# Kernel tuning notes

Measured on AMD Instinct MI355X. Metric: run time of the kernel, lower is better.

The kernel has to match this reference:

```python
import jax, jax.numpy as jnp
import numpy as np

NMS_THR = 0.7
TOPK = 128      # fixed post-NMS rois per level (static padding for jit)
OUT = 14        # RoIAlign output size
SAMPLES = 2     # samples per bin per dim (fixed approximation of sampling_ratio=-1)
STRIDES = (32.0, 16.0, 8.0)


def get_channel(a):
    # a: [..., 4] boxes as (cx, cy, w, h); FPN level assignment, clamped to [1, 4]
    s = jnp.sqrt(a[..., 2] * a[..., 3])
    return jnp.clip(jnp.floor(3.0 + jnp.log2(s / 224.0)), 1.0, 4.0)


def cxcywh_to_xyxy(b):
    cx, cy, w, h = b[..., 0], b[..., 1], b[..., 2], b[..., 3]
    return jnp.stack([cx - w / 2, cy - h / 2, cx + w / 2, cy + h / 2], axis=-1)


def pairwise_iou(b):
    x1, y1, x2, y2 = b[:, 0], b[:, 1], b[:, 2], b[:, 3]
    area = jnp.maximum(x2 - x1, 0.0) * jnp.maximum(y2 - y1, 0.0)
    ix1 = jnp.maximum(x1[:, None], x1[None, :])
    iy1 = jnp.maximum(y1[:, None], y1[None, :])
    ix2 = jnp.minimum(x2[:, None], x2[None, :])
    iy2 = jnp.minimum(y2[:, None], y2[None, :])
    inter = jnp.maximum(ix2 - ix1, 0.0) * jnp.maximum(iy2 - iy1, 0.0)
    union = area[:, None] + area[None, :] - inter
    return inter / jnp.maximum(union, 1e-9)


def nms_keep(boxes_xyxy, scores, thr):
    # Greedy NMS over masked scores (-inf entries sort last and are excluded later).
    n = scores.shape[0]
    order = jnp.argsort(-scores)
    iou = pairwise_iou(boxes_xyxy[order])  # [N, N]
    idx = jnp.arange(n)

    def body(sup, i):
        keep_i = ~sup[i]
        sup = sup | (keep_i & (iou[i] > thr) & (idx > i))
        return sup, keep_i

    _, keeps_sorted = jax.lax.scan(body, jnp.zeros(n, dtype=bool), idx)
    return jnp.zeros(n, dtype=bool).at[order].set(keeps_sorted)


def roi_align(feat, boxes):
    # feat: [C, H, W]; boxes: [K, 4]. NOTE: the original prepare_boxes feeds
    # (cx, cy, w, h) straight into RoIAlign, which interprets them as
    # (x1, y1, x2, y2) -- replicated faithfully here. spatial_scale = 1.
    C, H, W = feat.shape
    K = boxes.shape[0]
    x1, y1, x2, y2 = boxes[:, 0], boxes[:, 1], boxes[:, 2], boxes[:, 3]
    rw = jnp.maximum(x2 - x1, 1.0)
    rh = jnp.maximum(y2 - y1, 1.0)
    bw = rw / OUT
    bh = rh / OUT
    # fractional bin offsets, [OUT*SAMPLES]
    f = (jnp.arange(OUT, dtype=feat.dtype)[:, None]
         + (jnp.arange(SAMPLES, dtype=feat.dtype)[None, :] + 0.5) / SAMPLES).reshape(-1)
    ys = y1[:, None] + bh[:, None] * f[None, :]  # [K, S]
    xs = x1[:, None] + bw[:, None] * f[None, :]
    Y = ys[:, :, None]  # [K, S, 1]
    X = xs[:, None, :]  # [K, 1, S]
    valid = (Y > -1.0) & (Y < H) & (X > -1.0) & (X < W)  # [K, S, S]
    Yc = jnp.clip(Y, 0.0, H - 1.0)
    Xc = jnp.clip(X, 0.0, W - 1.0)
    y0 = jnp.floor(Yc)
    x0 = jnp.floor(Xc)
    y0i = y0.astype(jnp.int32)
    x0i = x0.astype(jnp.int32)
    y1i = jnp.minimum(y0i + 1, H - 1)
    x1i = jnp.minimum(x0i + 1, W - 1)
    ly = Yc - y0
    lx = Xc - x0
    hy = 1.0 - ly
    hx = 1.0 - lx
    g = lambda yi, xi: feat[:, yi, xi]  # -> [C, K, S, S]
    val = (g(y0i, x0i) * (hy * hx) + g(y0i, x1i) * (hy * lx)
           + g(y1i, x0i) * (ly * hx) + g(y1i, x1i) * (ly * lx))
    val = val * valid.astype(val.dtype)
    val = val.reshape(C, K, OUT, SAMPLES, OUT, SAMPLES).mean(axis=(3, 5))
    return jnp.transpose(val, (1, 0, 2, 3))  # [K, C, OUT, OUT]


def level_extract(feat, boxes, scores, levs, nl):
    # one image, one target FPN level: mask, NMS, fixed top-K select, RoIAlign
    mask = levs == nl
    msc = jnp.where(mask, scores, -jnp.inf)
    xyxy = cxcywh_to_xyxy(boxes)
    keep = nms_keep(jax.lax.stop_gradient(xyxy), jax.lax.stop_gradient(msc), NMS_THR)
    eff = jnp.where(keep & mask, msc, -jnp.inf)
    vals, sel = jax.lax.top_k(jax.lax.stop_gradient(eff), TOPK)
    valid = jnp.isfinite(vals)
    rois = boxes[sel] * valid[:, None].astype(boxes.dtype)
    out = roi_align(feat, rois)
    return out * valid[:, None, None, None].astype(out.dtype)


def _forward(p32, p16, p8, p4, a32, a16, a8, s32, s16, s8):
    anchors = (a32, a16, a8)  # p4 proposals are computed then discarded in the
    # original (grouping loop only runs l in range(3)); p4 features are never
    # RoIAligned either (nl loops 1..3), so p4 only appears as an unused input.
    levs = jnp.concatenate([get_channel(a) for a in anchors], axis=1)      # [B, N]
    boxes = jnp.concatenate([a * s for a, s in zip(anchors, STRIDES)], axis=1)
    scores = jnp.concatenate([s32, s16, s8], axis=1)
    outs = []
    for nl, feat in zip((1.0, 2.0, 3.0), (p32, p16, p8)):
        fn = jax.vmap(lambda f, b, s, l, nl=nl: level_extract(f, b, s, l, nl))
        outs.append(fn(feat, boxes, scores, levs))  # [B, TOPK, C, 14, 14]
    return jnp.concatenate(outs, axis=1)  # [B, 3*TOPK, C, 14, 14]


def setup_inputs():
    key = jax.random.key(0)
    ks = jax.random.split(key, 10)
    B, C = 2, 256
    p32 = jax.random.normal(ks[0], (B, C, 32, 32), jnp.float32)
    p16 = jax.random.normal(ks[1], (B, C, 64, 64), jnp.float32)
    p8 = jax.random.normal(ks[2], (B, C, 128, 128), jnp.float32)
    p4 = jax.random.normal(ks[3], (B, C, 256, 256), jnp.float32)

    def mk_anchors(k, n, hf):
        k1, k2 = jax.random.split(k)
        cxy = jax.random.uniform(k1, (B, n, 2), jnp.float32) * hf
        wh = 16.0 + jax.random.uniform(k2, (B, n, 2), jnp.float32) * 434.0
        return jnp.concatenate([cxy, wh], axis=-1)

    anchors_32 = mk_anchors(ks[4], 512, 32.0)
    anchors_16 = mk_anchors(ks[5], 1024, 64.0)
    anchors_8 = mk_anchors(ks[6], 2048, 128.0)
    scores_32 = jax.random.normal(ks[7], (B, 512), jnp.float32)
    scores_16 = jax.random.normal(ks[8], (B, 1024), jnp.float32)
    scores_8 = jax.random.normal(ks[9], (B, 2048), jnp.float32)
    return dict(p32=p32, p16=p16, p8=p8, p4=p4,
                anchors_32=anchors_32, anchors_16=anchors_16, anchors_8=anchors_8,
                scores_32=scores_32, scores_16=scores_16, scores_8=scores_8)


def reference(p32, p16, p8, p4, anchors_32, anchors_16, anchors_8,
              scores_32, scores_16, scores_8):
    return _forward(p32, p16, p8, p4, anchors_32, anchors_16, anchors_8,
                    scores_32, scores_16, scores_8)
```

## Files before the change

### kernel.cpp

```cpp
#include <hip/hip_runtime.h>
#include <stdint.h>

#define NMS_THR 0.7f
#define TOPK 128
#define NTOT 3584
#define CAP 2048
#define OUTSZ 14
#define NSAMP 28

typedef unsigned long long u64;
typedef float vf4 __attribute__((ext_vector_type(4)));
typedef float float2u __attribute__((ext_vector_type(2), aligned(4)));

__device__ __forceinline__ void fetch_anchor(
    const float* __restrict__ a32, const float* __restrict__ a16,
    const float* __restrict__ a8,
    const float* __restrict__ s32, const float* __restrict__ s16,
    const float* __restrict__ s8,
    int b, int i, float* A, float* st, float* sc)
{
    const float* P;
    if (i < 512) {
        P = a32 + (b * 512 + i) * 4;  *st = 32.0f; *sc = s32[b * 512 + i];
    } else if (i < 1536) {
        int j = i - 512;
        P = a16 + (b * 1024 + j) * 4; *st = 16.0f; *sc = s16[b * 1024 + j];
    } else {
        int j = i - 1536;
        P = a8 + (b * 2048 + j) * 4;  *st = 8.0f;  *sc = s8[b * 2048 + j];
    }
    float4 v = *(const float4*)P;
    A[0] = v.x; A[1] = v.y; A[2] = v.z; A[3] = v.w;
}

__global__ __launch_bounds__(1024) void select_kernel(
    const float* __restrict__ a32, const float* __restrict__ a16,
    const float* __restrict__ a8,
    const float* __restrict__ s32, const float* __restrict__ s16,
    const float* __restrict__ s8,
    float* __restrict__ rois,
    int* __restrict__ validOut)
{
    __shared__ u64 key[CAP];
    __shared__ float cbox[CAP * 5];
    __shared__ float kbox[TOPK * 5];
    __shared__ u64 supmat[64];
    __shared__ unsigned extf[64];
    __shared__ int selList[TOPK];
    __shared__ int mCount, keptSh;

    int prob = blockIdx.x;
    int b = prob / 3;
    int nl = prob % 3 + 1;
    int tid = threadIdx.x;

    if (tid == 0) { mCount = 0; keptSh = 0; }
    __syncthreads();

    for (int i = tid; i < NTOT; i += 1024) {
        float A[4], st, sc;
        fetch_anchor(a32, a16, a8, s32, s16, s8, b, i, A, &st, &sc);
        float s = sqrtf(__fmul_rn(A[2], A[3]));
        float lv = floorf(__fadd_rn(3.0f, log2f(__fdiv_rn(s, 224.0f))));
        lv = fminf(fmaxf(lv, 1.0f), 4.0f);
        if ((int)lv == nl) {
            unsigned u = __float_as_uint(sc);
            u = (u & 0x80000000u) ? ~u : (u | 0x80000000u);
            unsigned d = ~u;
            int pos = atomicAdd(&mCount, 1);
            if (pos < CAP) key[pos] = ((u64)d << 32) | (unsigned)i;
        }
    }
    __syncthreads();
    int m = mCount;
    if (m > CAP) m = CAP;
    int P2 = 64;
    while (P2 < m) P2 <<= 1;
    for (int i = m + tid; i < P2; i += 1024) key[i] = ~0ull;
    __syncthreads();

    for (int k = 2; k <= P2; k <<= 1) {
        for (int j = k >> 1; j > 0; j >>= 1) {
            for (int t = tid; t < P2; t += 1024) {
                int ixj = t ^ j;
                if (ixj > t) {
                    u64 a = key[t], bb = key[ixj];
                    bool up = ((t & k) == 0);
                    if ((a > bb) == up) { key[t] = bb; key[ixj] = a; }
                }
            }
            __syncthreads();
        }
    }

    for (int r = tid; r < m; r += 1024) {
        int orig = (int)(key[r] & 0xffffffffu);
        float A[4], st, sc;
        fetch_anchor(a32, a16, a8, s32, s16, s8, b, orig, A, &st, &sc);
        float cx = A[0] * st, cy = A[1] * st, w = A[2] * st, h = A[3] * st;
        float x1 = __fsub_rn(cx, 0.5f * w);
        float y1 = __fsub_rn(cy, 0.5f * h);
        float x2 = __fadd_rn(cx, 0.5f * w);
        float y2 = __fadd_rn(cy, 0.5f * h);
        cbox[r * 5 + 0] = x1; cbox[r * 5 + 1] = y1;
        cbox[r * 5 + 2] = x2; cbox[r * 5 + 3] = y2;
        cbox[r * 5 + 4] = __fmul_rn(fmaxf(__fsub_rn(x2, x1), 0.0f),
                                    fmaxf(__fsub_rn(y2, y1), 0.0f));
    }
    __syncthreads();

    int lane = tid & 63;
    int wv = tid >> 6;
    int kept = 0;

    for (int base = 0; base < m && kept < TOPK; base += 64) {
        int n = m - base; if (n > 64) n = 64;
        if (tid < 64) extf[tid] = 0;
        __syncthreads();

        bool cvalid = lane < n;
        int cidx = (base + (cvalid ? lane : 0)) * 5;
        float cx1 = cbox[cidx], cy1 = cbox[cidx + 1];
        float cx2 = cbox[cidx + 2], cy2 = cbox[cidx + 3], car = cbox[cidx + 4];

        for (int k = wv; k < kept; k += 16) {
            float kx1 = kbox[k * 5], ky1 = kbox[k * 5 + 1];
            float kx2 = kbox[k * 5 + 2], ky2 = kbox[k * 5 + 3], kar = kbox[k * 5 + 4];
            float i1 = fmaxf(kx1, cx1), i2 = fmaxf(ky1, cy1);
            float i3 = fminf(kx2, cx2), i4 = fminf(ky2, cy2);
            float inr = __fmul_rn(fmaxf(__fsub_rn(i3, i1), 0.0f),
                                  fmaxf(__fsub_rn(i4, i2), 0.0f));
            float unr = __fsub_rn(__fadd_rn(kar, car), inr);
            if (cvalid && __fdiv_rn(inr, fmaxf(unr, 1e-9f)) > NMS_THR)
                atomicOr(&extf[lane], 1u);
        }

        for (int r = 0; r < 4; r++) {
            int i = wv * 4 + r;
            u64 bal = 0;
            if (i < n) {
                int iidx = (base + i) * 5;
                float ix1 = cbox[iidx], iy1 = cbox[iidx + 1];
                float ix2 = cbox[iidx + 2], iy2 = cbox[iidx + 3], iar = cbox[iidx + 4];
                float i1 = fmaxf(ix1, cx1), i2 = fmaxf(iy1, cy1);
                float i3 = fminf(ix2, cx2), i4 = fminf(iy2, cy2);
                float inr = __fmul_rn(fmaxf(__fsub_rn(i3, i1), 0.0f),
                                      fmaxf(__fsub_rn(i4, i2), 0.0f));
                float unr = __fsub_rn(__fadd_rn(iar, car), inr);
                bool bit = cvalid && (lane > i) &&
                           (__fdiv_rn(inr, fmaxf(unr, 1e-9f)) > NMS_THR);
                bal = __ballot(bit);
            }
            if (lane == 0) supmat[i] = bal;
        }
        __syncthreads();

        if (wv == 0) {
            u64 row = supmat[lane];
            bool alive = (lane < n) && (extf[lane] == 0);
            int nk = kept;
            while (nk < TOPK) {
                u64 bal = __ballot(alive);
                if (bal == 0ull) break;
                int pick = __builtin_ctzll(bal);
                if (lane == 0) selList[nk] = base + pick;
                if (lane < 5) kbox[nk * 5 + lane] = cbox[(base + pick) * 5 + lane];
                int lo = __shfl((int)(unsigned)row, pick);
                int hi = __shfl((int)(row >> 32), pick);
                u64 prow = ((u64)(unsigned)hi << 32) | (unsigned)lo;
                alive = alive && !((prow >> lane) & 1ull) && (lane != pick);
                nk++;
            }
            if (lane == 0) keptSh = nk;
        }
        __syncthreads();
        kept = keptSh;
    }

    for (int k = tid; k < TOPK; k += 1024) {
        float4 rv = make_float4(0.0f, 0.0f, 0.0f, 0.0f);
        int vld = 0;
        if (k < kept) {
            int orig = (int)(key[selList[k]] & 0xffffffffu);
            float A[4], st, sc;
            fetch_anchor(a32, a16, a8, s32, s16, s8, b, orig, A, &st, &sc);
            rv = make_float4(A[0] * st, A[1] * st, A[2] * st, A[3] * st);
            vld = 1;
        }
        ((float4*)rois)[prob * TOPK + k] = rv;
        validOut[prob * TOPK + k] = vld;
    }
}

__global__ __launch_bounds__(256) void roialign_kernel(
    const float* __restrict__ p32, const float* __restrict__ p16,
    const float* __restrict__ p8,
    const float* __restrict__ rois, const int* __restrict__ validIn,
    float* __restrict__ out)
{
    int roiIdx = blockIdx.x;
    int b = roiIdx / 384;
    int slot = roiIdx - b * 384;
    int lvl = slot / TOPK;
    int k = slot - lvl * TOPK;
    int prob = b * 3 + lvl;
    int tid = threadIdx.x;

    float* O = out + (size_t)roiIdx * 256 * 196;

    vf4 z = (vf4)0.0f;
    vf4* O4 = (vf4*)O;
    for (int i = tid; i < 12544; i += 256) O4[i] = z;

    int vld = validIn[prob * TOPK + k];
    if (!vld) return;

    int W;
    const float* feat;
    if (lvl == 0)      { W = 32;  feat = p32; }
    else if (lvl == 1) { W = 64;  feat = p16; }
    else               { W = 128; feat = p8; }
    int HW = W * W;
    const float* F0 = feat + (size_t)b * 256 * HW;

    __shared__ int sxb[NSAMP], sy0[NSAMP], sy1[NSAMP];
    __shared__ float swx0[NSAMP], swx1[NSAMP], shy[NSAMP], sly[NSAMP];
    __shared__ int sxv[NSAMP], syv[NSAMP];
    __shared__ int oiL[OUTSZ], ojL[OUTSZ];
    __shared__ int nyx[2];

    if (tid < 2 * NSAMP) {
        const float* R = rois + ((size_t)prob * TOPK + k) * 4;
        float x1 = R[0], y1 = R[1], x2 = R[2], y2 = R[3];
        float rw = fmaxf(__fsub_rn(x2, x1), 1.0f);
        float rh = fmaxf(__fsub_rn(y2, y1), 1.0f);
        float bw = __fdiv_rn(rw, 14.0f);
        float bh = __fdiv_rn(rh, 14.0f);
        int axis = tid / NSAMP;
        int s = tid - axis * NSAMP;
        float fi = (float)(s >> 1) + ((s & 1) ? 0.75f : 0.25f);
        float start = axis ? y1 : x1;
        float bsz = axis ? bh : bw;
        float lim = (float)W;
        float X = __fadd_rn(start, __fmul_rn(bsz, fi));
        bool v = (X > -1.0f) && (X < lim);
        float Xc = fminf(fmaxf(X, 0.0f), lim - 1.0f);
        float x0f = floorf(Xc);
        int x0 = (int)x0f;
        float l = __fsub_rn(Xc, x0f);
        float hh = __fsub_rn(1.0f, l);
        float vf = v ? 1.0f : 0.0f;
        if (axis == 0) {
            int base; float w0, w1;
            if (x0 >= W - 1) { base = W - 2; w0 = 0.0f; w1 = vf; }
            else             { base = x0;    w0 = hh * vf; w1 = l * vf; }
            sxb[s] = base; swx0[s] = w0; swx1[s] = w1; sxv[s] = v ? 1 : 0;
        } else {
            sy0[s] = x0; sy1[s] = min(x0 + 1, W - 1);
            shy[s] = hh * vf; sly[s] = l * vf; syv[s] = v ? 1 : 0;
        }
    }
    __syncthreads();

    if (tid == 0) {
        int n = 0;
        for (int oi = 0; oi < OUTSZ; oi++)
            if (syv[2 * oi] | syv[2 * oi + 1]) oiL[n++] = oi;
        nyx[0] = n;
    }
    if (tid == 1) {
        int n = 0;
        for (int oj = 0; oj < OUTSZ; oj++)
            if (sxv[2 * oj] | sxv[2 * oj + 1]) ojL[n++] = oj;
        nyx[1] = n;
    }
    __syncthreads();

    int ny = nyx[0], nx = nyx[1];
    int total = ny * nx;
    if (total == 0) return;

    int w = tid >> 6;
    int lane = tid & 63;

    for (int ci = w; ci < total; ci += 4) {
        int oi = oiL[ci / nx];
        int oj = ojL[ci - (ci / nx) * nx];
        int sA = oi * 2, sB = sA + 1;
        int tA = oj * 2, tB = tA + 1;
        int y0A = sy0[sA], y1A = sy1[sA], y0B = sy0[sB], y1B = sy1[sB];
        float hyA = shy[sA], lyA = sly[sA], hyB = shy[sB], lyB = sly[sB];
        int xA = sxb[tA], xB = sxb[tB];
        float xw0A = swx0[tA], xw1A = swx1[tA];
        float xw0B = swx0[tB], xw1B = swx1[tB];
        int p = oi * 14 + oj;

        for (int it = 0; it < 4; it++) {
            int c = lane + it * 64;
            const float* F = F0 + c * HW;
            const float* rA0 = F + y0A * W;
            const float* rA1 = F + y1A * W;
            const float* rB0 = F + y0B * W;
            const float* rB1 = F + y1B * W;

            float2u a0 = *(const float2u*)(rA0 + xA);
            float2u a1 = *(const float2u*)(rA1 + xA);
            float2u c0 = *(const float2u*)(rA0 + xB);
            float2u c1 = *(const float2u*)(rA1 + xB);
            float2u b0 = *(const float2u*)(rB0 + xA);
            float2u b1 = *(const float2u*)(rB1 + xA);
            float2u d0 = *(const float2u*)(rB0 + xB);
            float2u d1 = *(const float2u*)(rB1 + xB);

            float s00 = hyA * (xw0A * a0.x + xw1A * a0.y) + lyA * (xw0A * a1.x + xw1A * a1.y);
            float s01 = hyA * (xw0B * c0.x + xw1B * c0.y) + lyA * (xw0B * c1.x + xw1B * c1.y);
            float s10 = hyB * (xw0A * b0.x + xw1A * b0.y) + lyB * (xw0A * b1.x + xw1A * b1.y);
            float s11 = hyB * (xw0B * d0.x + xw1B * d0.y) + lyB * (xw0B * d1.x + xw1B * d1.y);
            O[c * 196 + p] = 0.25f * (s00 + s01 + s10 + s11);
        }
    }
}

extern "C" void kernel_launch(void* const* d_in, const int* in_sizes, int n_in,
                              void* d_out, int out_size, void* d_ws, size_t ws_size,
                              hipStream_t stream) {
    const float* p32 = (const float*)d_in[0];
    const float* p16 = (const float*)d_in[1];
    const float* p8  = (const float*)d_in[2];
    const float* a32 = (const float*)d_in[4];
    const float* a16 = (const float*)d_in[5];
    const float* a8  = (const float*)d_in[6];
    const float* s32 = (const float*)d_in[7];
    const float* s16 = (const float*)d_in[8];
    const float* s8  = (const float*)d_in[9];
    float* out = (float*)d_out;

    const size_t totalFloats = 3072 + 768;

    float* base;
    if (ws_size >= totalFloats * 4) {
        base = (float*)d_ws;
    } else {
        base = (float*)d_in[3];
    }
    float* rois  = base;
    int*   valid = (int*)(base + 3072);

    select_kernel<<<6, 1024, 0, stream>>>(a32, a16, a8, s32, s16, s8,
                                          rois, valid);
    roialign_kernel<<<768, 256, 0, stream>>>(p32, p16, p8, rois, valid, out);
}
```

Measured before the change: 379.9 us.

## Overlap output zeroing with selection, precompute NMS suppression matrix, shuffle-based sort

The select kernel now launches 768 blocks. Blocks beyond the first six zero the whole output buffer while the six selection blocks run, and roialign no longer zeroes its slice first. The bitonic sort runs the small strides in registers with cross-lane shuffles, so fewer shared-memory barriers are needed. The full intra-chunk suppression bitmask for all 64-box chunks is computed in parallel before the greedy loop, and boxes are stored as float4, which cuts per-chunk sync and compute work. The cost is that the selection blocks now compete with the zeroing blocks for the GPU, and 768 blocks of 1024 threads each reserve the large shared-memory footprint.

```diff
diff --git a/kernel.cpp b/kernel.cpp
--- a/kernel.cpp
+++ b/kernel.cpp
@@ -7,10 +7,34 @@
 #define CAP 2048
 #define OUTSZ 14
 #define NSAMP 28
+#define OUT_VF4 (768 * 12544)
 
 typedef unsigned long long u64;
 typedef float vf4 __attribute__((ext_vector_type(4)));
 typedef float float2u __attribute__((ext_vector_type(2), aligned(4)));
+
+__device__ __forceinline__ u64 shfl_xor64(u64 v, int mask) {
+    int lo = __shfl_xor((int)(unsigned)v, mask);
+    int hi = __shfl_xor((int)(v >> 32), mask);
+    return ((u64)(unsigned)hi << 32) | (unsigned)lo;
+}
+__device__ __forceinline__ u64 shfl64(u64 v, int src) {
+    int lo = __shfl((int)(unsigned)v, src);
+    int hi = __shfl((int)(v >> 32), src);
+    return ((u64)(unsigned)hi << 32) | (unsigned)lo;
+}
+__device__ __forceinline__ void cex_shfl(u64 &e, int t, int j, int k) {
+    u64 p = shfl_xor64(e, j);
+    bool up = ((t & k) == 0);
+    bool lower = ((t & j) == 0);
+    u64 mn = (e < p) ? e : p;
+    u64 mx = (e < p) ? p : e;
+    e = (lower == up) ? mn : mx;
+}
+__device__ __forceinline__ float boxarea(float4 b) {
+    return __fmul_rn(fmaxf(__fsub_rn(b.z, b.x), 0.0f),
+                     fmaxf(__fsub_rn(b.w, b.y), 0.0f));
+}
 
 __device__ __forceinline__ void fetch_anchor(
     const float* __restrict__ a32, const float* __restrict__ a16,
@@ -39,22 +63,38 @@
     const float* __restrict__ s32, const float* __restrict__ s16,
     const float* __restrict__ s8,
     float* __restrict__ rois,
-    int* __restrict__ validOut)
+    int* __restrict__ validOut,
+    float* __restrict__ out)
 {
-    __shared__ u64 key[CAP];
-    __shared__ float cbox[CAP * 5];
-    __shared__ float kbox[TOPK * 5];
-    __shared__ u64 supmat[64];
-    __shared__ unsigned extf[64];
+    int tid = threadIdx.x;
+
+    if (blockIdx.x >= 6) {
+        vf4 z = (vf4)0.0f;
+        vf4* O4 = (vf4*)out;
+        int stride = (gridDim.x - 6) * 1024;
+        for (int i = (blockIdx.x - 6) * 1024 + tid; i < OUT_VF4; i += stride)
+            O4[i] = z;
+        return;
+    }
+
+    __shared__ u64 keysup[CAP];
+    __shared__ float4 cbox4[CAP];
+    __shared__ int sidx[CAP];
+    __shared__ float4 kb4[TOPK];
+    __shared__ float karea[TOPK];
+    __shared__ u64 extw[16];
     __shared__ int selList[TOPK];
     __shared__ int mCount, keptSh;
 
     int prob = blockIdx.x;
     int b = prob / 3;
     int nl = prob % 3 + 1;
-    int tid = threadIdx.x;
-
-    if (tid == 0) { mCount = 0; keptSh = 0; }
+    int lane = tid & 63;
+    int wv = tid >> 6;
+    int t0 = (wv << 7) + lane;
+    int t1 = t0 + 64;
+
+    if (tid == 0) mCount = 0;
     __syncthreads();
 
     for (int i = tid; i < NTOT; i += 1024) {
@@ -68,106 +108,132 @@
             u = (u & 0x80000000u) ? ~u : (u | 0x80000000u);
             unsigned d = ~u;
             int pos = atomicAdd(&mCount, 1);
-            if (pos < CAP) key[pos] = ((u64)d << 32) | (unsigned)i;
+            if (pos < CAP) keysup[pos] = ((u64)d << 32) | (unsigned)i;
         }
     }
     __syncthreads();
     int m = mCount;
     if (m > CAP) m = CAP;
-    int P2 = 64;
-    while (P2 < m) P2 <<= 1;
-    for (int i = m + tid; i < P2; i += 1024) key[i] = ~0ull;
-    __syncthreads();
-
-    for (int k = 2; k <= P2; k <<= 1) {
-        for (int j = k >> 1; j > 0; j >>= 1) {
-            for (int t = tid; t < P2; t += 1024) {
+    for (int i = m + tid; i < CAP; i += 1024) keysup[i] = ~0ull;
+    __syncthreads();
+
+    {
+        u64 e0 = keysup[t0], e1 = keysup[t1];
+        for (int k = 2; k <= 128; k <<= 1) {
+            int jstart = k >> 1;
+            if (k == 128) {
+                bool up = ((t0 & k) == 0);
+                if ((e0 > e1) == up) { u64 tmp = e0; e0 = e1; e1 = tmp; }
+                jstart = 32;
+            }
+            for (int j = jstart; j > 0; j >>= 1) {
+                cex_shfl(e0, t0, j, k);
+                cex_shfl(e1, t1, j, k);
+            }
+        }
+        keysup[t0] = e0; keysup[t1] = e1;
+    }
+    __syncthreads();
+    for (int k = 256; k <= 2048; k <<= 1) {
+        for (int j = k >> 1; j >= 128; j >>= 1) {
+            for (int t = tid; t < CAP; t += 1024) {
                 int ixj = t ^ j;
                 if (ixj > t) {
-                    u64 a = key[t], bb = key[ixj];
+                    u64 a = keysup[t], bb = keysup[ixj];
                     bool up = ((t & k) == 0);
-                    if ((a > bb) == up) { key[t] = bb; key[ixj] = a; }
+                    if ((a > bb) == up) { keysup[t] = bb; keysup[ixj] = a; }
                 }
             }
             __syncthreads();
         }
+        {
+            u64 e0 = keysup[t0], e1 = keysup[t1];
+            bool up = ((t0 & k) == 0);
+            if ((e0 > e1) == up) { u64 tmp = e0; e0 = e1; e1 = tmp; }
+            for (int j = 32; j > 0; j >>= 1) {
+                cex_shfl(e0, t0, j, k);
+                cex_shfl(e1, t1, j, k);
+            }
+            keysup[t0] = e0; keysup[t1] = e1;
+        }
+        __syncthreads();
     }
 
     for (int r = tid; r < m; r += 1024) {
-        int orig = (int)(key[r] & 0xffffffffu);
+        int orig = (int)(keysup[r] & 0xffffffffu);
+        sidx[r] = orig;
         float A[4], st, sc;
         fetch_anchor(a32, a16, a8, s32, s16, s8, b, orig, A, &st, &sc);
         float cx = A[0] * st, cy = A[1] * st, w = A[2] * st, h = A[3] * st;
-        float x1 = __fsub_rn(cx, 0.5f * w);
-        float y1 = __fsub_rn(cy, 0.5f * h);
-        float x2 = __fadd_rn(cx, 0.5f * w);
-        float y2 = __fadd_rn(cy, 0.5f * h);
-        cbox[r * 5 + 0] = x1; cbox[r * 5 + 1] = y1;
-        cbox[r * 5 + 2] = x2; cbox[r * 5 + 3] = y2;
-        cbox[r * 5 + 4] = __fmul_rn(fmaxf(__fsub_rn(x2, x1), 0.0f),
-                                    fmaxf(__fsub_rn(y2, y1), 0.0f));
-    }
-    __syncthreads();
-
-    int lane = tid & 63;
-    int wv = tid >> 6;
+        float4 v;
+        v.x = __fsub_rn(cx, 0.5f * w);
+        v.y = __fsub_rn(cy, 0.5f * h);
+        v.z = __fadd_rn(cx, 0.5f * w);
+        v.w = __fadd_rn(cy, 0.5f * h);
+        cbox4[r] = v;
+    }
+    __syncthreads();
+
+    int nch = (m + 63) >> 6;
+    for (int c = wv; c < nch; c += 16) {
+        int base = c << 6;
+        int n = m - base; if (n > 64) n = 64;
+        float4 cb = cbox4[base + ((lane < n) ? lane : 0)];
+        float car = boxarea(cb);
+        for (int i = 0; i < n; i++) {
+            float4 ib = cbox4[base + i];
+            float iar = boxarea(ib);
+            float i1 = fmaxf(ib.x, cb.x), i2 = fmaxf(ib.y, cb.y);
+            float i3 = fminf(ib.z, cb.z), i4 = fminf(ib.w, cb.w);
+            float inr = __fmul_rn(fmaxf(__fsub_rn(i3, i1), 0.0f),
+                                  fmaxf(__fsub_rn(i4, i2), 0.0f));
+            float unr = __fsub_rn(__fadd_rn(iar, car), inr);
+            bool bit = (lane < n) && (lane > i) &&
+                       (__fdiv_rn(inr, fmaxf(unr, 1e-9f)) > NMS_THR);
+            u64 bal = __ballot(bit);
+            if (lane == 0) keysup[base + i] = bal;
+        }
+    }
+    __syncthreads();
+
     int kept = 0;
-
-    for (int base = 0; base < m && kept < TOPK; base += 64) {
+    for (int c = 0; c < nch && kept < TOPK; c++) {
+        int base = c << 6;
         int n = m - base; if (n > 64) n = 64;
-        if (tid < 64) extf[tid] = 0;
-        __syncthreads();
-
-        bool cvalid = lane < n;
-        int cidx = (base + (cvalid ? lane : 0)) * 5;
-        float cx1 = cbox[cidx], cy1 = cbox[cidx + 1];
-        float cx2 = cbox[cidx + 2], cy2 = cbox[cidx + 3], car = cbox[cidx + 4];
-
-        for (int k = wv; k < kept; k += 16) {
-            float kx1 = kbox[k * 5], ky1 = kbox[k * 5 + 1];
-            float kx2 = kbox[k * 5 + 2], ky2 = kbox[k * 5 + 3], kar = kbox[k * 5 + 4];
-            float i1 = fmaxf(kx1, cx1), i2 = fmaxf(ky1, cy1);
-            float i3 = fminf(kx2, cx2), i4 = fminf(ky2, cy2);
+
+        float4 cb = cbox4[base + ((lane < n) ? lane : 0)];
+        float car = boxarea(cb);
+        bool s = false;
+        for (int kk = wv; kk < kept; kk += 16) {
+            float4 kb = kb4[kk]; float kar = karea[kk];
+            float i1 = fmaxf(kb.x, cb.x), i2 = fmaxf(kb.y, cb.y);
+            float i3 = fminf(kb.z, cb.z), i4 = fminf(kb.w, cb.w);
             float inr = __fmul_rn(fmaxf(__fsub_rn(i3, i1), 0.0f),
                                   fmaxf(__fsub_rn(i4, i2), 0.0f));
             float unr = __fsub_rn(__fadd_rn(kar, car), inr);
-            if (cvalid && __fdiv_rn(inr, fmaxf(unr, 1e-9f)) > NMS_THR)
-                atomicOr(&extf[lane], 1u);
-        }
-
-        for (int r = 0; r < 4; r++) {
-            int i = wv * 4 + r;
-            u64 bal = 0;
-            if (i < n) {
-                int iidx = (base + i) * 5;
-                float ix1 = cbox[iidx], iy1 = cbox[iidx + 1];
-                float ix2 = cbox[iidx + 2], iy2 = cbox[iidx + 3], iar = cbox[iidx + 4];
-                float i1 = fmaxf(ix1, cx1), i2 = fmaxf(iy1, cy1);
-                float i3 = fminf(ix2, cx2), i4 = fminf(iy2, cy2);
-                float inr = __fmul_rn(fmaxf(__fsub_rn(i3, i1), 0.0f),
-                                      fmaxf(__fsub_rn(i4, i2), 0.0f));
-                float unr = __fsub_rn(__fadd_rn(iar, car), inr);
-                bool bit = cvalid && (lane > i) &&
-                           (__fdiv_rn(inr, fmaxf(unr, 1e-9f)) > NMS_THR);
-                bal = __ballot(bit);
-            }
-            if (lane == 0) supmat[i] = bal;
-        }
+            if (__fdiv_rn(inr, fmaxf(unr, 1e-9f)) > NMS_THR) s = true;
+        }
+        u64 bal = __ballot(s);
+        if (lane == 0) extw[wv] = bal;
         __syncthreads();
 
         if (wv == 0) {
-            u64 row = supmat[lane];
-            bool alive = (lane < n) && (extf[lane] == 0);
+            u64 ext = 0;
+            #pragma unroll
+            for (int i = 0; i < 16; i++) ext |= extw[i];
+            u64 row = keysup[base + lane];
+            bool alive = (lane < n) && !((ext >> lane) & 1ull);
             int nk = kept;
             while (nk < TOPK) {
-                u64 bal = __ballot(alive);
-                if (bal == 0ull) break;
-                int pick = __builtin_ctzll(bal);
+                u64 b2 = __ballot(alive);
+                if (b2 == 0ull) break;
+                int pick = __builtin_ctzll(b2);
                 if (lane == 0) selList[nk] = base + pick;
-                if (lane < 5) kbox[nk * 5 + lane] = cbox[(base + pick) * 5 + lane];
-                int lo = __shfl((int)(unsigned)row, pick);
-                int hi = __shfl((int)(row >> 32), pick);
-                u64 prow = ((u64)(unsigned)hi << 32) | (unsigned)lo;
+                if (lane == 1) {
+                    float4 pb = cbox4[base + pick];
+                    kb4[nk] = pb; karea[nk] = boxarea(pb);
+                }
+                u64 prow = shfl64(row, pick);
                 alive = alive && !((prow >> lane) & 1ull) && (lane != pick);
                 nk++;
             }
@@ -181,7 +247,7 @@
         float4 rv = make_float4(0.0f, 0.0f, 0.0f, 0.0f);
         int vld = 0;
         if (k < kept) {
-            int orig = (int)(key[selList[k]] & 0xffffffffu);
+            int orig = sidx[selList[k]];
             float A[4], st, sc;
             fetch_anchor(a32, a16, a8, s32, s16, s8, b, orig, A, &st, &sc);
             rv = make_float4(A[0] * st, A[1] * st, A[2] * st, A[3] * st);
@@ -206,14 +272,10 @@
     int prob = b * 3 + lvl;
     int tid = threadIdx.x;
 
-    float* O = out + (size_t)roiIdx * 256 * 196;
-
-    vf4 z = (vf4)0.0f;
-    vf4* O4 = (vf4*)O;
-    for (int i = tid; i < 12544; i += 256) O4[i] = z;
-
     int vld = validIn[prob * TOPK + k];
     if (!vld) return;
+
+    float* O = out + (size_t)roiIdx * 256 * 196;
 
     int W;
     const float* feat;
@@ -346,7 +408,7 @@
     float* rois  = base;
     int*   valid = (int*)(base + 3072);
 
-    select_kernel<<<6, 1024, 0, stream>>>(a32, a16, a8, s32, s16, s8,
-                                          rois, valid);
+    select_kernel<<<768, 1024, 0, stream>>>(a32, a16, a8, s32, s16, s8,
+                                            rois, valid, out);
     roialign_kernel<<<768, 256, 0, stream>>>(p32, p16, p8, rois, valid, out);
 }
```

After: 362.1 us. 1.05x faster.
